# Performance work log

Measured on AMD Instinct MI355X. Metric: run time of the kernel, lower is better.

Reference implementation:

```python
import jax, jax.numpy as jnp
import numpy as np

B = 4096      # batch
N = 32768     # total tree nodes (real + pseudo classes) = columns of x
L = 12        # tree path depth (levels)
K = 64        # siblings (brother nodes) per level, padded to fixed width
C = 16384     # number of real classes (range of y)


def setup_inputs() -> dict:
    key = jax.random.key(0)
    k1, k2, k3, k4 = jax.random.split(key, 4)
    x = jax.random.normal(k1, (B, N), dtype=jnp.float32)
    # per-level sibling index sets (constants derived from the cover tree /
    # new2index / index2brother dicts in the original module)
    brother = jax.random.randint(k2, (L, K), 0, N)
    # the true path node at each level must be one of that level's siblings
    pos = jax.random.randint(k3, (L,), 0, K)
    p_y = brother[jnp.arange(L), pos]
    y = jax.random.randint(k4, (B,), 0, C)  # class labels (path selection baked into brother/p_y)
    return {"x": x, "brother": brother, "p_y": p_y, "y": y}


def reference(x, brother, p_y, y):
    # x: [B, N] logits over all tree nodes; brother: [L, K]; p_y: [L]
    gathered = x[:, brother]                      # [B, L, K] irregular column gather
    logp = jax.nn.log_softmax(gathered, axis=-1)  # per-level softmax over siblings
    # label = first position of the path node within its sibling set (torch nonzero()[0])
    labels = jnp.argmax(brother == p_y[:, None], axis=-1)          # [L]
    sel = jnp.take_along_axis(logp, labels[None, :, None], axis=2)[..., 0]  # [B, L]
    # CrossEntropyLoss = mean over batch of NLL, summed across tree levels
    return (-sel).mean(axis=0).sum()
```

## Files before the change

### kernel.cpp

```cpp
#include <hip/hip_runtime.h>

#define BB 4096
#define NN 32768
#define LL 12
#define KK 64
#define SS (LL * KK)

constexpr int TPB   = 256;
constexpr int NBLK  = 1024;
constexpr int RPB   = BB / NBLK;
constexpr int F4ROW = NN / 4;
constexpr int BATCH = 8;
constexpr int NWRD  = NN / 32;

#define LOADB(dst, rowp, bt) do {                                   \
    _Pragma("unroll")                                               \
    for (int u = 0; u < BATCH; ++u)                                 \
        dst[u] = (rowp)[((bt) * BATCH + u) * TPB + tid];            \
} while (0)

#define SCAT(src, bt) do {                                          \
    _Pragma("unroll")                                               \
    for (int u = 0; u < BATCH; ++u) {                               \
        const int fi = ((bt) * BATCH + u) * TPB + tid;              \
        const int wi = fi >> 3;                                     \
        const unsigned wrd = bmp[wi];                               \
        const int sh = (fi & 7) << 2;                               \
        const unsigned nib = (wrd >> sh) & 0xFu;                    \
        if (nib) {                                                  \
            int r = pfx[wi] + __popc(wrd & ((1u << sh) - 1u));      \
            if (nib & 1u) gath[r++] = src[u].x;                     \
            if (nib & 2u) gath[r++] = src[u].y;                     \
            if (nib & 4u) gath[r++] = src[u].z;                     \
            if (nib & 8u) gath[r++] = src[u].w;                     \
        }                                                           \
    }                                                               \
} while (0)

__global__ __launch_bounds__(TPB) void hsm_stream(
    const float* __restrict__ x,
    const int* __restrict__ brother,
    const int* __restrict__ p_y,
    float* __restrict__ partials) {

    __shared__ unsigned bmp[NWRD];
    __shared__ int      pfx[NWRD];
    __shared__ float    gath[SS];

    const int tid  = threadIdx.x;
    const int w    = tid >> 6;
    const int lane = tid & 63;

    const float4* xr = (const float4*)(x + (size_t)(blockIdx.x * RPB) * NN);
    float4 va[BATCH], vb[BATCH];
    LOADB(va, xr, 0);

    #pragma unroll
    for (int i = 0; i < NWRD / TPB; ++i) bmp[i * TPB + tid] = 0u;
    __syncthreads();

    int cols[3], label[3];
    #pragma unroll
    for (int j = 0; j < 3; ++j) {
        const int l = w + 4 * j;
        cols[j] = brother[l * KK + lane];
        label[j] = __ffsll(__ballot(cols[j] == p_y[l])) - 1;
        const int s = j * TPB + tid;
        atomicOr(&bmp[brother[s] >> 5], 1u << (brother[s] & 31));
    }
    __syncthreads();

    if (tid < 64) {
        int carry = 0;
        for (int c = 0; c < NWRD / 64; ++c) {
            const int v = __popc(bmp[c * 64 + tid]);
            int inc = v;
            #pragma unroll
            for (int o = 1; o < 64; o <<= 1) {
                const int t = __shfl_up(inc, o);
                if (tid >= o) inc += t;
            }
            pfx[c * 64 + tid] = carry + inc - v;
            carry += __shfl(inc, 63);
        }
    }
    __syncthreads();

    int dslot[3];
    #pragma unroll
    for (int j = 0; j < 3; ++j) {
        const int c = cols[j];
        dslot[j] = pfx[c >> 5] + __popc(bmp[c >> 5] & ((1u << (c & 31)) - 1u));
    }
    float acc[3] = {0.f, 0.f, 0.f};

    for (int r = 0; r < RPB; ++r) {
        LOADB(vb, xr, 1);
        SCAT(va, 0);
        LOADB(va, xr, 2);
        SCAT(vb, 1);
        LOADB(vb, xr, 3);
        SCAT(va, 2);
        const float4* xn = xr + F4ROW;
        if (r + 1 < RPB) LOADB(va, xn, 0);
        SCAT(vb, 3);
        __syncthreads();

        #pragma unroll
        for (int j = 0; j < 3; ++j) {
            const float vv = gath[dslot[j]];
            float mx = vv;
            #pragma unroll
            for (int o = 32; o > 0; o >>= 1) mx = fmaxf(mx, __shfl_xor(mx, o));
            float s = __expf(vv - mx);
            #pragma unroll
            for (int o = 32; o > 0; o >>= 1) s += __shfl_xor(s, o);
            acc[j] += mx + __logf(s) - __shfl(vv, label[j]);
        }
        __syncthreads();
        xr = xn;
    }

    if (lane == 0) {
        #pragma unroll
        for (int j = 0; j < 3; ++j)
            partials[(w + 4 * j) * NBLK + blockIdx.x] = acc[j];
    }
}

__global__ __launch_bounds__(256) void hsm_final(
    const float* __restrict__ partials, float* __restrict__ out) {
    const int w = threadIdx.x >> 6, lane = threadIdx.x & 63;
    __shared__ float red[LL];
    #pragma unroll
    for (int j = 0; j < 3; ++j) {
        const int l = w + 4 * j;
        float s = 0.f;
        for (int i = lane; i < NBLK; i += 64) s += partials[l * NBLK + i];
        #pragma unroll
        for (int o = 32; o > 0; o >>= 1) s += __shfl_xor(s, o);
        if (lane == 0) red[l] = s / (float)BB;
    }
    __syncthreads();
    if (threadIdx.x == 0) {
        float t = 0.f;
        #pragma unroll
        for (int i = 0; i < LL; ++i) t += red[i];
        out[0] = t;
    }
}

extern "C" void kernel_launch(void* const* d_in, const int* in_sizes, int n_in,
                              void* d_out, int out_size, void* d_ws, size_t ws_size,
                              hipStream_t stream) {
    const float* x       = (const float*)d_in[0];
    const int*   brother = (const int*)d_in[1];
    const int*   p_y     = (const int*)d_in[2];
    float* out      = (float*)d_out;
    float* partials = (float*)d_ws;

    hsm_stream<<<NBLK, TPB, 0, stream>>>(x, brother, p_y, partials);
    hsm_final<<<1, 256, 0, stream>>>(partials, out);
}
```

Baseline: 695.8 us.

## Split each row across two waves and parallelize bitmap prefix scan

Doubles the block count so each block handles two rows, with each wave streaming and scattering half of one row into a per-row shared gather buffer. The bitmap prefix sum, previously a serial loop in one wave, becomes a parallel scan across all four waves. Per-row, per-level losses go straight to a larger partials array that the final kernel reduces. This aims to raise parallelism and shorten per-block setup, at the cost of fewer loads in flight per lane and twice as many bitmap builds across blocks.

```diff
diff --git a/kernel.cpp b/kernel.cpp
--- a/kernel.cpp
+++ b/kernel.cpp
@@ -7,35 +7,10 @@
 #define SS (LL * KK)
 
 constexpr int TPB   = 256;
-constexpr int NBLK  = 1024;
-constexpr int RPB   = BB / NBLK;
-constexpr int F4ROW = NN / 4;
-constexpr int BATCH = 8;
+constexpr int NBLK  = 2048;
 constexpr int NWRD  = NN / 32;
-
-#define LOADB(dst, rowp, bt) do {                                   \
-    _Pragma("unroll")                                               \
-    for (int u = 0; u < BATCH; ++u)                                 \
-        dst[u] = (rowp)[((bt) * BATCH + u) * TPB + tid];            \
-} while (0)
-
-#define SCAT(src, bt) do {                                          \
-    _Pragma("unroll")                                               \
-    for (int u = 0; u < BATCH; ++u) {                               \
-        const int fi = ((bt) * BATCH + u) * TPB + tid;              \
-        const int wi = fi >> 3;                                     \
-        const unsigned wrd = bmp[wi];                               \
-        const int sh = (fi & 7) << 2;                               \
-        const unsigned nib = (wrd >> sh) & 0xFu;                    \
-        if (nib) {                                                  \
-            int r = pfx[wi] + __popc(wrd & ((1u << sh) - 1u));      \
-            if (nib & 1u) gath[r++] = src[u].x;                     \
-            if (nib & 2u) gath[r++] = src[u].y;                     \
-            if (nib & 4u) gath[r++] = src[u].z;                     \
-            if (nib & 8u) gath[r++] = src[u].w;                     \
-        }                                                           \
-    }                                                               \
-} while (0)
+constexpr int HF4   = NN / 4 / 2;
+constexpr int NB    = HF4 / 64 / 4;
 
 __global__ __launch_bounds__(TPB) void hsm_stream(
     const float* __restrict__ x,
@@ -45,86 +20,116 @@
 
     __shared__ unsigned bmp[NWRD];
     __shared__ int      pfx[NWRD];
-    __shared__ float    gath[SS];
+    __shared__ float    gath[2][SS];
+    __shared__ int      strip[4];
 
     const int tid  = threadIdx.x;
     const int w    = tid >> 6;
     const int lane = tid & 63;
-
-    const float4* xr = (const float4*)(x + (size_t)(blockIdx.x * RPB) * NN);
-    float4 va[BATCH], vb[BATCH];
-    LOADB(va, xr, 0);
+    const int rloc = w >> 1;
+    const int half = w & 1;
+    const int row  = blockIdx.x * 2 + rloc;
 
     #pragma unroll
     for (int i = 0; i < NWRD / TPB; ++i) bmp[i * TPB + tid] = 0u;
     __syncthreads();
-
-    int cols[3], label[3];
     #pragma unroll
-    for (int j = 0; j < 3; ++j) {
-        const int l = w + 4 * j;
-        cols[j] = brother[l * KK + lane];
-        label[j] = __ffsll(__ballot(cols[j] == p_y[l])) - 1;
-        const int s = j * TPB + tid;
-        atomicOr(&bmp[brother[s] >> 5], 1u << (brother[s] & 31));
+    for (int j = 0; j < SS / TPB; ++j) {
+        const int c = brother[j * TPB + tid];
+        atomicOr(&bmp[c >> 5], 1u << (c & 31));
     }
     __syncthreads();
 
-    if (tid < 64) {
-        int carry = 0;
-        for (int c = 0; c < NWRD / 64; ++c) {
-            const int v = __popc(bmp[c * 64 + tid]);
-            int inc = v;
-            #pragma unroll
-            for (int o = 1; o < 64; o <<= 1) {
-                const int t = __shfl_up(inc, o);
-                if (tid >= o) inc += t;
-            }
-            pfx[c * 64 + tid] = carry + inc - v;
-            carry += __shfl(inc, 63);
+    {
+        const int base = w * 256 + lane * 4;
+        int c0 = __popc(bmp[base]), c1 = __popc(bmp[base + 1]);
+        int c2 = __popc(bmp[base + 2]), c3 = __popc(bmp[base + 3]);
+        const int tot = c0 + c1 + c2 + c3;
+        int incl = tot;
+        #pragma unroll
+        for (int o = 1; o < 64; o <<= 1) {
+            const int t = __shfl_up(incl, o);
+            if (lane >= o) incl += t;
+        }
+        if (lane == 63) strip[w] = incl;
+        __syncthreads();
+        int run = incl - tot;
+        for (int j = 0; j < w; ++j) run += strip[j];
+        pfx[base] = run;  run += c0;
+        pfx[base + 1] = run; run += c1;
+        pfx[base + 2] = run; run += c2;
+        pfx[base + 3] = run;
+    }
+    __syncthreads();
+
+    const int   sh  = (lane & 7) << 2;
+    const unsigned msk = (1u << sh) - 1u;
+    const float4* xh = (const float4*)(x + (size_t)row * NN) + half * HF4;
+    float* g = gath[rloc];
+    const int wbase = half * (NWRD / 2);
+
+#define LOAD4(buf, bt) do {                                         \
+    _Pragma("unroll")                                               \
+    for (int u = 0; u < 4; ++u)                                     \
+        buf[u] = xh[(((bt) * 4 + u) * 64) + lane];                  \
+} while (0)
+
+#define SCAT4(buf, bt) do {                                         \
+    _Pragma("unroll")                                               \
+    for (int u = 0; u < 4; ++u) {                                   \
+        const int bi = (bt) * 4 + u;                                \
+        const int wi = wbase + bi * 8 + (lane >> 3);                \
+        const unsigned wrd = bmp[wi];                               \
+        const unsigned nib = (wrd >> sh) & 0xFu;                    \
+        if (nib) {                                                  \
+            int r = pfx[wi] + __popc(wrd & msk);                    \
+            if (nib & 1u) g[r++] = buf[u].x;                        \
+            if (nib & 2u) g[r++] = buf[u].y;                        \
+            if (nib & 4u) g[r++] = buf[u].z;                        \
+            if (nib & 8u) g[r]   = buf[u].w;                        \
+        }                                                           \
+    }                                                               \
+} while (0)
+
+    {
+        float4 va[4], vb[4];
+        LOAD4(va, 0);
+        #pragma unroll 1
+        for (int it = 0; it < NB; it += 2) {
+            LOAD4(vb, it + 1);
+            SCAT4(va, it);
+            if (it + 2 < NB) LOAD4(va, it + 2);
+            SCAT4(vb, it + 1);
         }
     }
     __syncthreads();
 
-    int dslot[3];
+    int colv[LL / 2];
     #pragma unroll
-    for (int j = 0; j < 3; ++j) {
-        const int c = cols[j];
-        dslot[j] = pfx[c >> 5] + __popc(bmp[c >> 5] & ((1u << (c & 31)) - 1u));
+    for (int j = 0; j < LL / 2; ++j)
+        colv[j] = brother[(half * (LL / 2) + j) * KK + lane];
+
+    float my = 0.f;
+    #pragma unroll
+    for (int j = 0; j < LL / 2; ++j) {
+        const int l  = half * (LL / 2) + j;
+        const int c  = colv[j];
+        const int lab = __ffsll(__ballot(c == p_y[l])) - 1;
+        const unsigned wrd = bmp[c >> 5];
+        const int ds = pfx[c >> 5] + __popc(wrd & ((1u << (c & 31)) - 1u));
+        const float vv = g[ds];
+        float mx = vv;
+        #pragma unroll
+        for (int o = 32; o > 0; o >>= 1) mx = fmaxf(mx, __shfl_xor(mx, o));
+        float s = __expf(vv - mx);
+        #pragma unroll
+        for (int o = 32; o > 0; o >>= 1) s += __shfl_xor(s, o);
+        const float loss = mx + __logf(s) - __shfl(vv, lab);
+        if (lane == l) my = loss;
     }
-    float acc[3] = {0.f, 0.f, 0.f};
-
-    for (int r = 0; r < RPB; ++r) {
-        LOADB(vb, xr, 1);
-        SCAT(va, 0);
-        LOADB(va, xr, 2);
-        SCAT(vb, 1);
-        LOADB(vb, xr, 3);
-        SCAT(va, 2);
-        const float4* xn = xr + F4ROW;
-        if (r + 1 < RPB) LOADB(va, xn, 0);
-        SCAT(vb, 3);
-        __syncthreads();
-
-        #pragma unroll
-        for (int j = 0; j < 3; ++j) {
-            const float vv = gath[dslot[j]];
-            float mx = vv;
-            #pragma unroll
-            for (int o = 32; o > 0; o >>= 1) mx = fmaxf(mx, __shfl_xor(mx, o));
-            float s = __expf(vv - mx);
-            #pragma unroll
-            for (int o = 32; o > 0; o >>= 1) s += __shfl_xor(s, o);
-            acc[j] += mx + __logf(s) - __shfl(vv, label[j]);
-        }
-        __syncthreads();
-        xr = xn;
-    }
-
-    if (lane == 0) {
-        #pragma unroll
-        for (int j = 0; j < 3; ++j)
-            partials[(w + 4 * j) * NBLK + blockIdx.x] = acc[j];
+    if ((lane >> 3) == 0 || true) {
+        if (lane >= half * (LL / 2) && lane < half * (LL / 2) + LL / 2)
+            partials[lane * BB + row] = my;
     }
 }
 
@@ -136,7 +141,7 @@
     for (int j = 0; j < 3; ++j) {
         const int l = w + 4 * j;
         float s = 0.f;
-        for (int i = lane; i < NBLK; i += 64) s += partials[l * NBLK + i];
+        for (int i = lane; i < BB; i += 64) s += partials[l * BB + i];
         #pragma unroll
         for (int o = 32; o > 0; o >>= 1) s += __shfl_xor(s, o);
         if (lane == 0) red[l] = s / (float)BB;
```

After: 733.7 us. 5.5% more time.
